# Kernel optimization log

Measured on AMD Instinct MI355X. Metric: run time of the kernel, lower is better.

## Reference

```python
import jax, jax.numpy as jnp
import numpy as np

N_QUBITS = 10
DEPTH = 5
NUM_CLASSES = 2
DIM = 2 ** N_QUBITS  # 1024


def _rx(t):
    # RX(t) = [[cos(t/2), -i sin(t/2)], [-i sin(t/2), cos(t/2)]]
    c, s = jnp.cos(t / 2), jnp.sin(t / 2)
    zr = jnp.zeros_like(t)
    a = jax.lax.complex(c, zr)
    b = jax.lax.complex(zr, -s)
    return jnp.stack([jnp.stack([a, b]), jnp.stack([b, a])]).astype(jnp.complex64)


def _rz(t):
    # RZ(t) = diag(e^{-it/2}, e^{it/2})
    c, s = jnp.cos(t / 2), jnp.sin(t / 2)
    e = jax.lax.complex(c, -s)
    z = jnp.zeros_like(e)
    return jnp.stack([jnp.stack([e, z]), jnp.stack([z, jnp.conj(e)])]).astype(jnp.complex64)


def _apply_1q(state, U, wire):
    # state: (B, 2, ..., 2); wire axis is wire+1 (wire 0 = most significant bit)
    s = jnp.moveaxis(state, wire + 1, -1)
    s = s @ U.T
    return jnp.moveaxis(s, -1, wire + 1)


def _apply_c1q(state, U, ctrl, tgt):
    # controlled-U: apply U on tgt where ctrl qubit is |1>
    s = jnp.moveaxis(state, ctrl + 1, 1)  # (B, 2_ctrl, rest...)
    ax = tgt + 1 if tgt < ctrl else tgt   # tgt axis inside s[:, k]
    s1 = s[:, 1]
    s1 = jnp.moveaxis(s1, ax, -1) @ U.T
    s1 = jnp.moveaxis(s1, -1, ax)
    s = jnp.stack([s[:, 0], s1], axis=1)
    return jnp.moveaxis(s, 1, ctrl + 1)


def _circuit(x, weights, weights_1, weights_2):
    B = x.shape[0]
    x = x.reshape(B, -1)
    x = jnp.pad(x, ((0, 0), (0, DIM - x.shape[1])))  # pad_with=0
    x = x / jnp.linalg.norm(x, axis=1, keepdims=True)  # normalize=True
    state = jax.lax.complex(x, jnp.zeros_like(x)).reshape((B,) + (2,) * N_QUBITS)
    for d in range(DEPTH):
        for i in range(N_QUBITS):
            state = _apply_1q(state, _rx(weights[d, i, 0]), i)
            state = _apply_1q(state, _rz(weights[d, i, 1]), i)
            state = _apply_1q(state, _rx(weights[d, i, 2]), i)
        r = 1 if d % 2 == 0 else 3  # alternating entangler range (CCQC)
        for i in range(N_QUBITS):
            c = (i + r) % N_QUBITS
            state = _apply_c1q(state, _rz(weights[d, i, 3]), c, i)
            state = _apply_c1q(state, _rx(weights[d, i, 4]), c, i)
        state = _apply_1q(state, _rx(weights_1[d]), 0)
        state = _apply_1q(state, _rz(weights_2[d]), 0)
    probs = (jnp.abs(state) ** 2).reshape(B, DIM)
    # <Z_w> signs: bit w (MSB-first) of each basis index
    bits = (jnp.arange(DIM)[None, :] >> (N_QUBITS - 1 - jnp.arange(N_QUBITS)[:, None])) & 1
    zsign = (1 - 2 * bits).astype(probs.dtype)  # (n_qubits, DIM)
    return probs @ zsign.T  # (B, n_qubits)


def setup_inputs() -> dict:
    key = jax.random.key(0)
    ks = jax.random.split(key, 5)
    B = 8192
    x = jax.random.normal(ks[0], (B, 784), dtype=jnp.float32)
    y = jax.random.randint(ks[1], (B,), 0, NUM_CLASSES)
    weights = jax.random.uniform(ks[2], (DEPTH, N_QUBITS, 5), jnp.float32, 0.0, 2 * np.pi)
    weights_1 = jax.random.uniform(ks[3], (DEPTH,), jnp.float32, 0.0, 2 * np.pi)
    weights_2 = jax.random.uniform(ks[4], (DEPTH,), jnp.float32, 0.0, 2 * np.pi)
    return {"x": x, "y": y, "weights": weights, "weights_1": weights_1, "weights_2": weights_2}


def reference(x, y, weights, weights_1, weights_2):
    expz = _circuit(x, weights, weights_1, weights_2)
    logits = expz[:, :NUM_CLASSES]
    logp = jax.nn.log_softmax(logits, axis=-1)
    nll = -jnp.take_along_axis(logp, y[:, None].astype(jnp.int32), axis=1)[:, 0]
    return jnp.mean(nll)  # CrossEntropyLoss (mean reduction)
```

## Files before the change

### kernel.cpp

```cpp
#include <hip/hip_runtime.h>


namespace {

typedef float f32x2 __attribute__((ext_vector_type(2)));
typedef __fp16 fp16x2 __attribute__((ext_vector_type(2)));
typedef _Float16 f16x8 __attribute__((ext_vector_type(8)));
typedef float f32x4v __attribute__((ext_vector_type(4)));

__device__ __forceinline__ f32x2 pk_mul(f32x2 a, f32x2 b) {
  f32x2 d;
  asm("v_pk_mul_f32 %0, %1, %2" : "=v"(d) : "v"(a), "v"(b));
  return d;
}
__device__ __forceinline__ f32x2 pk_fma(f32x2 a, f32x2 b, f32x2 c) {
  f32x2 d;
  asm("v_pk_fma_f32 %0, %1, %2, %3" : "=v"(d) : "v"(a), "v"(b), "v"(c));
  return d;
}
__device__ __forceinline__ f32x2 pk_fma_swap1(f32x2 a, f32x2 b, f32x2 c) {
  f32x2 d;
  asm("v_pk_fma_f32 %0, %1, %2, %3 op_sel:[0,1,0] op_sel_hi:[1,0,1]"
      : "=v"(d) : "v"(a), "v"(b), "v"(c));
  return d;
}
__device__ __forceinline__ f32x2 cmulp(f32x2 cr2, f32x2 ci2, f32x2 v) {
  return pk_fma_swap1(ci2, v, pk_mul(cr2, v));
}
__device__ __forceinline__ f32x2 cmad(f32x2 acc, f32x2 cr2, f32x2 ci2, f32x2 v) {
  return pk_fma_swap1(ci2, v, pk_fma(cr2, v, acc));
}

__device__ __forceinline__ f32x2 shfl_xor2(f32x2 v, int lm) {
  f32x2 r;
  r.x = __shfl_xor(v.x, lm, 64);
  r.y = __shfl_xor(v.y, lm, 64);
  return r;
}
template <int CTRL>
__device__ __forceinline__ f32x2 dpp_xor2(f32x2 v) {
  f32x2 r;
  const int ix = __builtin_bit_cast(int, v.x);
  const int iy = __builtin_bit_cast(int, v.y);
  r.x = __builtin_bit_cast(float,
      __builtin_amdgcn_update_dpp(0, ix, CTRL, 0xF, 0xF, true));
  r.y = __builtin_bit_cast(float,
      __builtin_amdgcn_update_dpp(0, iy, CTRL, 0xF, 0xF, true));
  return r;
}
__device__ __forceinline__ f32x2 shfl_fast(f32x2 v, const int lm) {
  if (lm == 1) return dpp_xor2<0xB1>(v);
  if (lm == 2) return dpp_xor2<0x4E>(v);
  return shfl_xor2(v, lm);
}

struct c2 { float r, i; };
struct m2c { c2 a00, a01, a10, a11; };

__device__ __forceinline__ c2 cmul(c2 x, c2 y) { return {x.r*y.r - x.i*y.i, x.r*y.i + x.i*y.r}; }
__device__ __forceinline__ c2 cadd(c2 x, c2 y) { return {x.r + y.r, x.i + y.i}; }
__device__ __forceinline__ c2 conjc(c2 a) { return {a.r, -a.i}; }
__device__ __forceinline__ m2c mmul(m2c A, m2c B) {
  m2c C;
  C.a00 = cadd(cmul(A.a00, B.a00), cmul(A.a01, B.a10));
  C.a01 = cadd(cmul(A.a00, B.a01), cmul(A.a01, B.a11));
  C.a10 = cadd(cmul(A.a10, B.a00), cmul(A.a11, B.a10));
  C.a11 = cadd(cmul(A.a10, B.a01), cmul(A.a11, B.a11));
  return C;
}
__device__ __forceinline__ m2c madj(m2c U) {
  return { conjc(U.a00), conjc(U.a10), conjc(U.a01), conjc(U.a11) };
}
__device__ __forceinline__ m2c mrx(float t) {
  float c = cosf(0.5f * t), s = sinf(0.5f * t);
  return { {c, 0.f}, {0.f, -s}, {0.f, -s}, {c, 0.f} };
}
__device__ __forceinline__ m2c mrz(float t) {
  float c = cosf(0.5f * t), s = sinf(0.5f * t);
  return { {c, -s}, {0.f, 0.f}, {0.f, 0.f}, {c, s} };
}

__device__ __forceinline__ bool fusable(int d, int i) {
  return (d & 1) ? (i >= 3) : (i >= 1);
}

__global__ void make_prog(const float* __restrict__ w, const float* __restrict__ w1,
                          const float* __restrict__ w2, float* __restrict__ prog,
                          float* __restrict__ outp) {
  const int t = threadIdx.x;
  if (t == 127) outp[0] = 0.f;
  int kind = -1, od = 0, oi = 0, p = 0;
  for (int dd = 0; dd < 5; ++dd) {
    const int d = 4 - dd;
    if (d == 4) { if (p == t) kind = 0; ++p; }
    for (int ii = 0; ii < 10; ++ii) {
      const int i = 9 - ii;
      if (p == t) { kind = (d <= 3 && fusable(d, i)) ? 2 : 1; od = d; oi = i; }
      ++p;
    }
    for (int ii = 0; ii < 10; ++ii) {
      const int i = 9 - ii;
      if (d >= 1 && fusable(d - 1, i)) continue;
      if (p == t) { kind = 3; od = d; oi = i; }
      ++p;
    }
  }
  if (kind < 0) return;

  auto u1mat = [&](int d, int i) -> m2c {
    const float* pw = w + (d * 10 + i) * 5;
    m2c U = mmul(mrx(pw[2]), mmul(mrz(pw[1]), mrx(pw[0])));
    if (i == 0 && d > 0) {
      m2c U0 = mmul(mrz(w2[d - 1]), mrx(w1[d - 1]));
      U = mmul(U, U0);
    }
    return U;
  };
  auto cumat = [&](int d, int i) -> m2c {
    const float* pw = w + (d * 10 + i) * 5;
    return mmul(mrx(pw[4]), mrz(pw[3]));
  };

  m2c M0{}, M1{};
  int bt = 9;
  if (kind == 0) {
    M0 = madj(mmul(mrz(w2[4]), mrx(w1[4]))); M1 = M0; bt = 9;
  } else if (kind == 1) {
    M1 = madj(cumat(od, oi));
    M0 = m2c{ {1.f, 0.f}, {0.f, 0.f}, {0.f, 0.f}, {1.f, 0.f} };
    bt = 9 - oi;
  } else if (kind == 2) {
    m2c V1 = madj(u1mat(od + 1, oi));
    m2c VC = madj(cumat(od, oi));
    M0 = V1; M1 = mmul(VC, V1);
    bt = 9 - oi;
  } else {
    M0 = madj(u1mat(od, oi)); M1 = M0; bt = 9 - oi;
  }

  float* o = prog + t * 64;
  if (bt >= 8) {
    const m2c* Ms[2] = {&M0, &M1};
    #pragma unroll
    for (int c = 0; c < 2; ++c) {
      const c2 e[4] = {Ms[c]->a00, Ms[c]->a01, Ms[c]->a10, Ms[c]->a11};
      #pragma unroll
      for (int q = 0; q < 4; ++q) {
        o[c*16 + q*4 + 0] = e[q].r; o[c*16 + q*4 + 1] = e[q].r;
        o[c*16 + q*4 + 2] = -e[q].i; o[c*16 + q*4 + 3] = e[q].i;
      }
    }
  } else {
    #pragma unroll
    for (int v = 0; v < 4; ++v) {
      const bool hi = (v & 1) != 0;
      const m2c& M = (v >> 1) ? M1 : M0;
      const c2 cA = hi ? M.a11 : M.a00;
      const c2 cB = hi ? M.a10 : M.a01;
      o[v*8+0] = cA.r; o[v*8+1] = cA.r; o[v*8+2] = -cA.i; o[v*8+3] = cA.i;
      o[v*8+4] = cB.r; o[v*8+5] = cB.r; o[v*8+6] = -cB.i; o[v*8+7] = cB.i;
    }
  }
}

struct CoefP { f32x2 Ar, Ai, Br, Bi; };
__device__ __forceinline__ CoefP ldcoef(const float* __restrict__ g, int v) {
  const float4* p = reinterpret_cast<const float4*>(g + v * 8);
  const float4 a = p[0], b = p[1];
  return { f32x2{a.x, a.y}, f32x2{a.z, a.w}, f32x2{b.x, b.y}, f32x2{b.z, b.w} };
}
struct MatP { f32x2 u00r, u00i, u01r, u01i, u10r, u10i, u11r, u11i; };
__device__ __forceinline__ MatP ldmat16(const float* __restrict__ g, int c) {
  const float4* p = reinterpret_cast<const float4*>(g + c * 16);
  const float4 a = p[0], b = p[1], cc = p[2], d = p[3];
  MatP m;
  m.u00r = f32x2{a.x, a.y};  m.u00i = f32x2{a.z, a.w};
  m.u01r = f32x2{b.x, b.y};  m.u01i = f32x2{b.z, b.w};
  m.u10r = f32x2{cc.x, cc.y}; m.u10i = f32x2{cc.z, cc.w};
  m.u11r = f32x2{d.x, d.y};  m.u11i = f32x2{d.z, d.w};
  return m;
}
__device__ __forceinline__ f32x2 capply(const CoefP& c, f32x2 own, f32x2 par) {
  return cmad(cmulp(c.Ar, c.Ai, own), c.Br, c.Bi, par);
}
__device__ __forceinline__ void mat_pair(const MatP& m, f32x2& a, f32x2& b) {
  const f32x2 na = cmad(cmulp(m.u00r, m.u00i, a), m.u01r, m.u01i, b);
  const f32x2 nb = cmad(cmulp(m.u10r, m.u10i, a), m.u11r, m.u11i, b);
  a = na; b = nb;
}

__device__ __forceinline__ void apply_op(f32x2 (&sA)[4], f32x2 (&sB)[4],
                                         f32x2* lxb, const int wv,
                                         const int lane, const float* __restrict__ g,
                                         const int bt, const int bc) {
  if (bt >= 8) {
    const int tm = 1 << (bt - 8);
    if (bc >= 8) {
      const int cb = bc - 8;
      const MatP m0 = ldmat16(g, 0), m1 = ldmat16(g, 1);
      #pragma unroll
      for (int k0 = 0; k0 < 4; ++k0) {
        if (k0 & tm) continue;
        const int k1 = k0 | tm;
        const MatP& m = ((k0 >> cb) & 1) ? m1 : m0;
        mat_pair(m, sA[k0], sA[k1]);
        mat_pair(m, sB[k0], sB[k1]);
      }
    } else {
      int c = 0;
      if (bc >= 6)      c = (wv >> (bc - 6)) & 1;
      else if (bc >= 0) c = (lane >> bc) & 1;
      const MatP m = ldmat16(g, c);
      #pragma unroll
      for (int k0 = 0; k0 < 4; ++k0) {
        if (k0 & tm) continue;
        const int k1 = k0 | tm;
        mat_pair(m, sA[k0], sA[k1]);
        mat_pair(m, sB[k0], sB[k1]);
      }
    }
  } else if (bt >= 6) {
    const int tb = bt - 6;
    const int hi = (wv >> tb) & 1;
    #pragma unroll
    for (int k = 0; k < 4; ++k) {
      lxb[(wv * 4 + k) * 64 + lane] = sA[k];
      lxb[1024 + (wv * 4 + k) * 64 + lane] = sB[k];
    }
    __syncthreads();
    const int pw = wv ^ (1 << tb);
    f32x2 pA[4], pB[4];
    #pragma unroll
    for (int k = 0; k < 4; ++k) {
      pA[k] = lxb[(pw * 4 + k) * 64 + lane];
      pB[k] = lxb[1024 + (pw * 4 + k) * 64 + lane];
    }
    if (bc >= 8) {
      const int cb = bc - 8;
      const CoefP c0 = ldcoef(g, hi), c1 = ldcoef(g, hi + 2);
      #pragma unroll
      for (int k = 0; k < 4; ++k) {
        const CoefP& cf = ((k >> cb) & 1) ? c1 : c0;
        sA[k] = capply(cf, sA[k], pA[k]);
        sB[k] = capply(cf, sB[k], pB[k]);
      }
    } else {
      int c = 0;
      if (bc >= 6)      c = (wv >> (bc - 6)) & 1;
      else if (bc >= 0) c = (lane >> bc) & 1;
      const CoefP cf = ldcoef(g, hi + 2 * c);
      #pragma unroll
      for (int k = 0; k < 4; ++k) {
        sA[k] = capply(cf, sA[k], pA[k]);
        sB[k] = capply(cf, sB[k], pB[k]);
      }
    }
  } else {
    const int lm = 1 << bt;
    const int hi = (lane >> bt) & 1;
    if (bc >= 8) {
      const int cb = bc - 8;
      const CoefP c0 = ldcoef(g, hi), c1 = ldcoef(g, hi + 2);
      #pragma unroll
      for (int k = 0; k < 4; ++k) {
        const CoefP& cf = ((k >> cb) & 1) ? c1 : c0;
        const f32x2 pA = shfl_fast(sA[k], lm);
        const f32x2 pB = shfl_fast(sB[k], lm);
        sA[k] = capply(cf, sA[k], pA);
        sB[k] = capply(cf, sB[k], pB);
      }
    } else {
      int c = 0;
      if (bc >= 6)      c = (wv >> (bc - 6)) & 1;
      else if (bc >= 0) c = (lane >> bc) & 1;
      const CoefP cf = ldcoef(g, hi + 2 * c);
      #pragma unroll
      for (int k = 0; k < 4; ++k) {
        const f32x2 pA = shfl_fast(sA[k], lm);
        const f32x2 pB = shfl_fast(sB[k], lm);
        sA[k] = capply(cf, sA[k], pA);
        sB[k] = capply(cf, sB[k], pB);
      }
    }
  }
}

__global__ __launch_bounds__(256) void qprep(const float* __restrict__ prog,
                                             const float* __restrict__ x,
                                             _Float16* __restrict__ Wt,
                                             _Float16* __restrict__ Xh) {
  const int tid = threadIdx.x;
  if (blockIdx.x >= 512) {
    const int t = (blockIdx.x - 512) * 256 + tid;
    const int b = t >> 7;
    const int j = (t & 127) * 8;
    if (j >= 832) return;
    union { fp16x2 h2[4]; f16x8 h8; } u;
    if (j < 784) {
      const float4* p = reinterpret_cast<const float4*>(x + (size_t)b * 784 + j);
      const float4 v0 = p[0], v1 = p[1];
      u.h2[0] = __builtin_amdgcn_cvt_pkrtz(v0.x, v0.y);
      u.h2[1] = __builtin_amdgcn_cvt_pkrtz(v0.z, v0.w);
      u.h2[2] = __builtin_amdgcn_cvt_pkrtz(v1.x, v1.y);
      u.h2[3] = __builtin_amdgcn_cvt_pkrtz(v1.z, v1.w);
    } else {
      #pragma unroll
      for (int q = 0; q < 4; ++q) u.h2[q] = __builtin_amdgcn_cvt_pkrtz(0.f, 0.f);
    }
    *reinterpret_cast<f16x8*>(Xh + (size_t)b * 1024 + j) = u.h8;
    return;
  }

  __shared__ f32x2 lx[2][2048];

  const int lane = tid & 63;
  const int wv = tid >> 6;
  const int n0 = blockIdx.x * 2;
  const int n1 = n0 + 1;

  f32x2 sA[4], sB[4];
  #pragma unroll
  for (int k = 0; k < 4; ++k) {
    const int j = (k << 8) | (wv << 6) | lane;
    sA[k].x = (j == n0) ? 1.f : 0.f; sA[k].y = 0.f;
    sB[k].x = (j == n1) ? 1.f : 0.f; sB[k].y = 0.f;
  }

  int p = 0, ph = 0;
  #pragma unroll
  for (int dd = 0; dd < 5; ++dd) {
    const int d = 4 - dd;
    if (d == 4) {
      apply_op(sA, sB, &lx[ph & 1][0], wv, lane, prog + p * 64, 9, -1);
      ++p;
    }
    const int r = (d & 1) ? 3 : 1;
    #pragma unroll
    for (int ii = 0; ii < 10; ++ii) {
      const int i = 9 - ii;
      const int c = (i + r) % 10;
      const int bt = 9 - i, bc = 9 - c;
      apply_op(sA, sB, &lx[ph & 1][0], wv, lane, prog + p * 64, bt, bc);
      ++p; if (bt >= 6 && bt < 8) ++ph;
    }
    #pragma unroll
    for (int ii = 0; ii < 10; ++ii) {
      const int i = 9 - ii;
      if (d >= 1 && fusable(d - 1, i)) continue;
      const int bt = 9 - i;
      apply_op(sA, sB, &lx[ph & 1][0], wv, lane, prog + p * 64, bt, -1);
      ++p; if (bt >= 6 && bt < 8) ++ph;
    }
  }

  #pragma unroll
  for (int k = 0; k < 4; ++k) {
    const int j = (k << 8) | (wv << 6) | lane;
    Wt[(size_t)(2 * n0) * 1024 + j] = (_Float16)sA[k].x;
    Wt[(size_t)(2 * n0 + 1) * 1024 + j] = (_Float16)(-sA[k].y);
    Wt[(size_t)(2 * n1) * 1024 + j] = (_Float16)sB[k].x;
    Wt[(size_t)(2 * n1 + 1) * 1024 + j] = (_Float16)(-sB[k].y);
  }
}

#define GZ_NSTEP 13

__device__ __forceinline__ void stage_tiles(const _Float16* __restrict__ gA,
                                            const _Float16* __restrict__ gB,
                                            _Float16* sA, _Float16* sB,
                                            int k0, int wv, int lane) {
  const int rIn = lane >> 3;
  const int colh = ((lane & 7) ^ rIn) * 8;
  #pragma unroll
  for (int c = 0; c < 2; ++c) {
    const int chunk = wv * 2 + c;
    const size_t grow = (size_t)(chunk * 8 + rIn) * 1024 + k0 + colh;
    auto* la = (__attribute__((address_space(3))) void*)(sA + chunk * 512 + lane * 8);
    __builtin_amdgcn_global_load_lds(
        (const __attribute__((address_space(1))) void*)(gA + grow), la, 16, 0, 0);
    auto* lb = (__attribute__((address_space(3))) void*)(sB + chunk * 512 + lane * 8);
    __builtin_amdgcn_global_load_lds(
        (const __attribute__((address_space(1))) void*)(gB + grow), lb, 16, 0, 0);
  }
}

__device__ __forceinline__ int lds_off(int row, int slot) {
  return row * 64 + ((slot ^ (row & 7)) * 8);
}

__global__ __launch_bounds__(512) void gemm_z(const _Float16* __restrict__ Xh,
                                              const _Float16* __restrict__ Wt,
                                              float* __restrict__ part, int B) {
  __shared__ _Float16 smA[2][128 * 64];
  __shared__ _Float16 smB[2][128 * 64];

  const int tid = threadIdx.x;
  const int lane = tid & 63;
  const int wv = tid >> 6;
  const int wm = wv >> 1;
  const int wn = wv & 1;
  const int row0 = blockIdx.x * 128;
  const int n0 = blockIdx.y * 128;

  const _Float16* gA = Xh + (size_t)row0 * 1024;
  const _Float16* gB = Wt + (size_t)n0 * 1024;

  const int lr = lane & 15;
  const int lq = lane >> 4;

  f32x4v acc[2][4];
  #pragma unroll
  for (int m = 0; m < 2; ++m)
    #pragma unroll
    for (int f = 0; f < 4; ++f) acc[m][f] = f32x4v{0.f, 0.f, 0.f, 0.f};

  stage_tiles(gA, gB, smA[0], smB[0], 0, wv, lane);
  __syncthreads();

  for (int t = 0; t < GZ_NSTEP; ++t) {
    const int cur = t & 1;
    if (t + 1 < GZ_NSTEP)
      stage_tiles(gA, gB, smA[cur ^ 1], smB[cur ^ 1], (t + 1) * 64, wv, lane);

    #pragma unroll
    for (int kk = 0; kk < 2; ++kk) {
      const int slot = kk * 4 + lq;
      f16x8 a[2], b[4];
      #pragma unroll
      for (int m = 0; m < 2; ++m) {
        const int row = wm * 32 + m * 16 + lr;
        a[m] = *reinterpret_cast<const f16x8*>(&smA[cur][lds_off(row, slot)]);
      }
      #pragma unroll
      for (int f = 0; f < 4; ++f) {
        const int row = wn * 64 + f * 16 + lr;
        b[f] = *reinterpret_cast<const f16x8*>(&smB[cur][lds_off(row, slot)]);
      }
      #pragma unroll
      for (int m = 0; m < 2; ++m)
        #pragma unroll
        for (int f = 0; f < 4; ++f)
          acc[m][f] = __builtin_amdgcn_mfma_f32_16x16x32_f16(a[m], b[f], acc[m][f], 0, 0, 0);
    }
    __syncthreads();
  }

  const int pp = blockIdx.y * 2 + wn;
  #pragma unroll
  for (int m = 0; m < 2; ++m) {
    f32x4v p = f32x4v{0.f, 0.f, 0.f, 0.f};
    #pragma unroll
    for (int f = 0; f < 4; ++f) p += acc[m][f] * acc[m][f];
    #pragma unroll
    for (int msk = 1; msk < 16; msk <<= 1) {
      p.x += __shfl_xor(p.x, msk, 64);
      p.y += __shfl_xor(p.y, msk, 64);
      p.z += __shfl_xor(p.z, msk, 64);
      p.w += __shfl_xor(p.w, msk, 64);
    }
    if (lr == 0) {
      const int rbase = row0 + wm * 32 + m * 16 + lq * 4;
      float* dst = part + (size_t)pp * B + rbase;
      dst[0] = p.x; dst[1] = p.y; dst[2] = p.z; dst[3] = p.w;
    }
  }
}

__global__ __launch_bounds__(256) void nll_part(const float* __restrict__ part,
                                                const int* __restrict__ y,
                                                float* __restrict__ out, int B,
                                                float scale) {
  const int row = blockIdx.x * 256 + threadIdx.x;
  float q0 = 0.f, q1 = 0.f, nn = 0.f;
  #pragma unroll
  for (int pp = 0; pp < 32; ++pp) {
    const float P = part[(size_t)pp * B + row];
    q0 += (pp & 16) ? -P : P;
    q1 += (pp & 8) ? -P : P;
    nn += P;
  }
  const float z0 = q0 / nn, z1 = q1 / nn;
  const float mx = fmaxf(z0, z1);
  const float lse = mx + logf(expf(z0 - mx) + expf(z1 - mx));
  const float ly = (y[row] == 0) ? z0 : z1;
  float s = lse - ly;
  #pragma unroll
  for (int msk = 1; msk < 64; msk <<= 1) s += __shfl_xor(s, msk, 64);
  __shared__ float red[4];
  if ((threadIdx.x & 63) == 0) red[threadIdx.x >> 6] = s;
  __syncthreads();
  if (threadIdx.x == 0)
    atomicAdd(out, (red[0] + red[1] + red[2] + red[3]) * scale);
}

}

extern "C" void kernel_launch(void* const* d_in, const int* in_sizes, int n_in,
                              void* d_out, int out_size, void* d_ws, size_t ws_size,
                              hipStream_t stream) {
  const float* x  = (const float*)d_in[0];
  const int*   y  = (const int*)d_in[1];
  const float* w  = (const float*)d_in[2];
  const float* w1 = (const float*)d_in[3];
  const float* w2 = (const float*)d_in[4];
  float* out = (float*)d_out;

  const int B = in_sizes[0] / 784;

  char* ws = (char*)d_ws;
  _Float16* Wt   = (_Float16*)ws;
  _Float16* Xh   = (_Float16*)(ws + (size_t)2048 * 1024 * 2);
  float*    part = (float*)(ws + (size_t)2048 * 1024 * 2 + (size_t)B * 1024 * 2);
  float*    prog = part + (size_t)32 * B;

  make_prog<<<1, 128, 0, stream>>>(w, w1, w2, prog, out);
  qprep<<<512 + (B * 128) / 256, 256, 0, stream>>>(prog, x, Wt, Xh);
  gemm_z<<<dim3(B / 128, 16), 512, 0, stream>>>(Xh, Wt, part, B);
  nll_part<<<B / 256, 256, 0, stream>>>(part, y, out, B, 1.0f / (float)B);
}
```

Measured before the change: 75.37 us.

## Simulate one basis state per 128-thread block with 8 amplitudes per thread

The qprep kernel now evolves a single basis column per block using 2 waves of 64 lanes, each holding 8 register amplitudes, instead of two columns per 4-wave block with 4 amplitudes each. Qubits with bit position 7 and above become in-register pair updates, so only bit 6 needs an LDS exchange with a barrier, where before bits 6 and 7 both did. The goal is fewer __syncthreads and less LDS traffic per gate, plus twice as many smaller blocks. The cost is higher register pressure per thread. The x-to-fp16 conversion path is also re-mapped so each block handles one row.

```diff
diff --git a/kernel.cpp b/kernel.cpp
--- a/kernel.cpp
+++ b/kernel.cpp
@@ -139,7 +139,7 @@
   }
 
   float* o = prog + t * 64;
-  if (bt >= 8) {
+  if (bt >= 7) {
     const m2c* Ms[2] = {&M0, &M1};
     #pragma unroll
     for (int c = 0; c < 2; ++c) {
@@ -189,111 +189,91 @@
   a = na; b = nb;
 }
 
-__device__ __forceinline__ void apply_op(f32x2 (&sA)[4], f32x2 (&sB)[4],
-                                         f32x2* lxb, const int wv,
+__device__ __forceinline__ void apply_op(f32x2 (&s)[8], f32x2* lxb, const int wv,
                                          const int lane, const float* __restrict__ g,
                                          const int bt, const int bc) {
-  if (bt >= 8) {
-    const int tm = 1 << (bt - 8);
-    if (bc >= 8) {
-      const int cb = bc - 8;
+  if (bt >= 7) {
+    const int tm = 1 << (bt - 7);
+    if (bc >= 7) {
+      const int cb = bc - 7;
       const MatP m0 = ldmat16(g, 0), m1 = ldmat16(g, 1);
       #pragma unroll
-      for (int k0 = 0; k0 < 4; ++k0) {
+      for (int k0 = 0; k0 < 8; ++k0) {
         if (k0 & tm) continue;
         const int k1 = k0 | tm;
         const MatP& m = ((k0 >> cb) & 1) ? m1 : m0;
-        mat_pair(m, sA[k0], sA[k1]);
-        mat_pair(m, sB[k0], sB[k1]);
+        mat_pair(m, s[k0], s[k1]);
       }
     } else {
       int c = 0;
-      if (bc >= 6)      c = (wv >> (bc - 6)) & 1;
+      if (bc == 6)      c = wv;
       else if (bc >= 0) c = (lane >> bc) & 1;
       const MatP m = ldmat16(g, c);
       #pragma unroll
-      for (int k0 = 0; k0 < 4; ++k0) {
+      for (int k0 = 0; k0 < 8; ++k0) {
         if (k0 & tm) continue;
         const int k1 = k0 | tm;
-        mat_pair(m, sA[k0], sA[k1]);
-        mat_pair(m, sB[k0], sB[k1]);
-      }
-    }
-  } else if (bt >= 6) {
-    const int tb = bt - 6;
-    const int hi = (wv >> tb) & 1;
-    #pragma unroll
-    for (int k = 0; k < 4; ++k) {
-      lxb[(wv * 4 + k) * 64 + lane] = sA[k];
-      lxb[1024 + (wv * 4 + k) * 64 + lane] = sB[k];
-    }
+        mat_pair(m, s[k0], s[k1]);
+      }
+    }
+  } else if (bt == 6) {
+    const int hi = wv;
+    #pragma unroll
+    for (int k = 0; k < 8; ++k) lxb[(wv * 8 + k) * 64 + lane] = s[k];
     __syncthreads();
-    const int pw = wv ^ (1 << tb);
-    f32x2 pA[4], pB[4];
-    #pragma unroll
-    for (int k = 0; k < 4; ++k) {
-      pA[k] = lxb[(pw * 4 + k) * 64 + lane];
-      pB[k] = lxb[1024 + (pw * 4 + k) * 64 + lane];
-    }
-    if (bc >= 8) {
-      const int cb = bc - 8;
+    const int pw = wv ^ 1;
+    f32x2 pp[8];
+    #pragma unroll
+    for (int k = 0; k < 8; ++k) pp[k] = lxb[(pw * 8 + k) * 64 + lane];
+    if (bc >= 7) {
+      const int cb = bc - 7;
       const CoefP c0 = ldcoef(g, hi), c1 = ldcoef(g, hi + 2);
       #pragma unroll
-      for (int k = 0; k < 4; ++k) {
+      for (int k = 0; k < 8; ++k) {
         const CoefP& cf = ((k >> cb) & 1) ? c1 : c0;
-        sA[k] = capply(cf, sA[k], pA[k]);
-        sB[k] = capply(cf, sB[k], pB[k]);
+        s[k] = capply(cf, s[k], pp[k]);
       }
     } else {
       int c = 0;
-      if (bc >= 6)      c = (wv >> (bc - 6)) & 1;
-      else if (bc >= 0) c = (lane >> bc) & 1;
+      if (bc >= 0) c = (lane >> bc) & 1;
       const CoefP cf = ldcoef(g, hi + 2 * c);
       #pragma unroll
-      for (int k = 0; k < 4; ++k) {
-        sA[k] = capply(cf, sA[k], pA[k]);
-        sB[k] = capply(cf, sB[k], pB[k]);
-      }
+      for (int k = 0; k < 8; ++k) s[k] = capply(cf, s[k], pp[k]);
     }
   } else {
     const int lm = 1 << bt;
     const int hi = (lane >> bt) & 1;
-    if (bc >= 8) {
-      const int cb = bc - 8;
+    if (bc >= 7) {
+      const int cb = bc - 7;
       const CoefP c0 = ldcoef(g, hi), c1 = ldcoef(g, hi + 2);
       #pragma unroll
-      for (int k = 0; k < 4; ++k) {
+      for (int k = 0; k < 8; ++k) {
         const CoefP& cf = ((k >> cb) & 1) ? c1 : c0;
-        const f32x2 pA = shfl_fast(sA[k], lm);
-        const f32x2 pB = shfl_fast(sB[k], lm);
-        sA[k] = capply(cf, sA[k], pA);
-        sB[k] = capply(cf, sB[k], pB);
+        const f32x2 p = shfl_fast(s[k], lm);
+        s[k] = capply(cf, s[k], p);
       }
     } else {
       int c = 0;
-      if (bc >= 6)      c = (wv >> (bc - 6)) & 1;
+      if (bc == 6)      c = wv;
       else if (bc >= 0) c = (lane >> bc) & 1;
       const CoefP cf = ldcoef(g, hi + 2 * c);
       #pragma unroll
-      for (int k = 0; k < 4; ++k) {
-        const f32x2 pA = shfl_fast(sA[k], lm);
-        const f32x2 pB = shfl_fast(sB[k], lm);
-        sA[k] = capply(cf, sA[k], pA);
-        sB[k] = capply(cf, sB[k], pB);
-      }
-    }
-  }
-}
-
-__global__ __launch_bounds__(256) void qprep(const float* __restrict__ prog,
+      for (int k = 0; k < 8; ++k) {
+        const f32x2 p = shfl_fast(s[k], lm);
+        s[k] = capply(cf, s[k], p);
+      }
+    }
+  }
+}
+
+__global__ __launch_bounds__(128) void qprep(const float* __restrict__ prog,
                                              const float* __restrict__ x,
                                              _Float16* __restrict__ Wt,
                                              _Float16* __restrict__ Xh) {
   const int tid = threadIdx.x;
-  if (blockIdx.x >= 512) {
-    const int t = (blockIdx.x - 512) * 256 + tid;
-    const int b = t >> 7;
-    const int j = (t & 127) * 8;
+  if (blockIdx.x >= 1024) {
+    const int b = blockIdx.x - 1024;
+    const int j = tid * 8;
     if (j >= 832) return;
     union { fp16x2 h2[4]; f16x8 h8; } u;
     if (j < 784) {
@@ -311,19 +291,18 @@
     return;
   }
 
-  __shared__ f32x2 lx[2][2048];
+  __shared__ f32x2 lx[2][1024];
 
   const int lane = tid & 63;
   const int wv = tid >> 6;
-  const int n0 = blockIdx.x * 2;
-  const int n1 = n0 + 1;
-
-  f32x2 sA[4], sB[4];
-  #pragma unroll
-  for (int k = 0; k < 4; ++k) {
-    const int j = (k << 8) | (wv << 6) | lane;
-    sA[k].x = (j == n0) ? 1.f : 0.f; sA[k].y = 0.f;
-    sB[k].x = (j == n1) ? 1.f : 0.f; sB[k].y = 0.f;
+  const int n = blockIdx.x;
+
+  f32x2 s[8];
+  #pragma unroll
+  for (int k = 0; k < 8; ++k) {
+    const int j = (k << 7) | (wv << 6) | lane;
+    s[k].x = (j == n) ? 1.f : 0.f;
+    s[k].y = 0.f;
   }
 
   int p = 0, ph = 0;
@@ -331,7 +310,7 @@
   for (int dd = 0; dd < 5; ++dd) {
     const int d = 4 - dd;
     if (d == 4) {
-      apply_op(sA, sB, &lx[ph & 1][0], wv, lane, prog + p * 64, 9, -1);
+      apply_op(s, &lx[ph & 1][0], wv, lane, prog + p * 64, 9, -1);
       ++p;
     }
     const int r = (d & 1) ? 3 : 1;
@@ -340,26 +319,24 @@
       const int i = 9 - ii;
       const int c = (i + r) % 10;
       const int bt = 9 - i, bc = 9 - c;
-      apply_op(sA, sB, &lx[ph & 1][0], wv, lane, prog + p * 64, bt, bc);
-      ++p; if (bt >= 6 && bt < 8) ++ph;
+      apply_op(s, &lx[ph & 1][0], wv, lane, prog + p * 64, bt, bc);
+      ++p; if (bt == 6) ++ph;
     }
     #pragma unroll
     for (int ii = 0; ii < 10; ++ii) {
       const int i = 9 - ii;
       if (d >= 1 && fusable(d - 1, i)) continue;
       const int bt = 9 - i;
-      apply_op(sA, sB, &lx[ph & 1][0], wv, lane, prog + p * 64, bt, -1);
-      ++p; if (bt >= 6 && bt < 8) ++ph;
-    }
-  }
-
-  #pragma unroll
-  for (int k = 0; k < 4; ++k) {
-    const int j = (k << 8) | (wv << 6) | lane;
-    Wt[(size_t)(2 * n0) * 1024 + j] = (_Float16)sA[k].x;
-    Wt[(size_t)(2 * n0 + 1) * 1024 + j] = (_Float16)(-sA[k].y);
-    Wt[(size_t)(2 * n1) * 1024 + j] = (_Float16)sB[k].x;
-    Wt[(size_t)(2 * n1 + 1) * 1024 + j] = (_Float16)(-sB[k].y);
+      apply_op(s, &lx[ph & 1][0], wv, lane, prog + p * 64, bt, -1);
+      ++p; if (bt == 6) ++ph;
+    }
+  }
+
+  #pragma unroll
+  for (int k = 0; k < 8; ++k) {
+    const int j = (k << 7) | (wv << 6) | lane;
+    Wt[(size_t)(2 * n) * 1024 + j] = (_Float16)s[k].x;
+    Wt[(size_t)(2 * n + 1) * 1024 + j] = (_Float16)(-s[k].y);
   }
 }
 
@@ -514,7 +491,7 @@
   float*    prog = part + (size_t)32 * B;
 
   make_prog<<<1, 128, 0, stream>>>(w, w1, w2, prog, out);
-  qprep<<<512 + (B * 128) / 256, 256, 0, stream>>>(prog, x, Wt, Xh);
+  qprep<<<1024 + B, 128, 0, stream>>>(prog, x, Wt, Xh);
   gemm_z<<<dim3(B / 128, 16), 512, 0, stream>>>(Xh, Wt, part, B);
   nll_part<<<B / 256, 256, 0, stream>>>(part, y, out, B, 1.0f / (float)B);
 }
```

Result: no change. 74.06 us, median of 2 (-1.7%).
